# Kernel tuning notes

Hardware: AMD Instinct MI355X
Metric: run time of the kernel (lower is better)

Reference implementation:

```python
import jax, jax.numpy as jnp
import numpy as np

B, N, D = 8, 256, 64  # batch, n_entities, feature dim


def setup_inputs() -> dict:
    key = jax.random.key(0)
    ks = jax.random.split(key, 8)
    s = 0.02
    return {
        "emb1": jax.random.normal(ks[0], (B, N, D), jnp.float32),
        "emb2": jax.random.normal(ks[1], (B, N, N, D), jnp.float32),
        "W1a": jax.random.normal(ks[2], (3 * D, 128), jnp.float32) * s,
        "b1a": jnp.zeros((128,), jnp.float32),
        "W1b": jax.random.normal(ks[3], (128, D), jnp.float32) * s,
        "b1b": jnp.zeros((D,), jnp.float32),
        "W2a": jax.random.normal(ks[4], (4 * D, 256), jnp.float32) * s,
        "b2a": jnp.zeros((256,), jnp.float32),
        "W2b": jax.random.normal(ks[5], (256, D), jnp.float32) * s,
        "b2b": jnp.zeros((D,), jnp.float32),
    }


def _mlp(x, Wa, ba, Wb, bb):
    h = jax.nn.relu(jnp.einsum("...i,io->...o", x, Wa) + ba)
    return jnp.einsum("...i,io->...o", h, Wb) + bb


def reference(emb1, emb2, W1a, b1a, W1b, b1b, W2a, b2a, W2b, b2b):
    # arity 1: reduce arity-2 embedding over second entity dim (max & min), concat
    red_max = jnp.max(emb2, axis=-2)           # [B,N,D]
    red_min = jnp.min(emb2, axis=-2)           # [B,N,D]
    cat1 = jnp.concatenate([emb1, red_max, red_min], axis=-1)  # [B,N,3D]

    # arity 2: expand arity-1 embedding along a new entity dim, concat with emb2
    exp = jnp.broadcast_to(emb1[:, :, None, :], emb2.shape)    # [B,N,N,D]
    cat2 = jnp.concatenate([exp, emb2], axis=-1)               # [B,N,N,2D]

    # permutation gather: position (i,j) gets [cat2[j,i], cat2[i,j]] along features
    perm2 = jnp.concatenate([jnp.transpose(cat2, (0, 2, 1, 3)), cat2], axis=-1)  # [B,N,N,4D]

    out1 = _mlp(cat1, W1a, b1a, W1b, b1b)    # [B,N,D]
    out2 = _mlp(perm2, W2a, b2a, W2b, b2b)   # [B,N,N,D]
    return (out1, out2)
```

## Files before the change

### kernel.cpp

```cpp
#include <hip/hip_runtime.h>
#include <hip/hip_bf16.h>

typedef __bf16 bf16x8 __attribute__((ext_vector_type(8)));
typedef float f32x4 __attribute__((ext_vector_type(4)));
typedef unsigned int u32;
typedef unsigned short u16;
typedef u32 u32x4 __attribute__((ext_vector_type(4)));
typedef u16 u16x4 __attribute__((ext_vector_type(4)));
typedef u16 u16x8 __attribute__((ext_vector_type(8)));

__device__ __forceinline__ u16 f2bf(float x) {
  u32 u = __float_as_uint(x);
  return (u16)((u + 0x7FFFu + ((u >> 16) & 1u)) >> 16);
}
__device__ __forceinline__ u16 cvt_bf16(float x) {
  __bf16 h = (__bf16)x;
  return __builtin_bit_cast(u16, h);
}
__device__ __forceinline__ float bf2f(u16 h) {
  return __uint_as_float((u32)h << 16);
}

__device__ __forceinline__ bf16x8 ld_frag_lds(const u16* base, int byteOff) {
  u32x4 v = *(const u32x4*)((const char*)base + byteOff);
  return __builtin_bit_cast(bf16x8, v);
}
__device__ __forceinline__ bf16x8 ld_frag_glb(const u16* p) {
  u32x4 v = *(const u32x4*)p;
  return __builtin_bit_cast(bf16x8, v);
}

__global__ void prep_w_kernel(const float* __restrict__ W2a, const float* __restrict__ W2b,
                              u16* __restrict__ wfA, u16* __restrict__ wfB2) {
  int t = blockIdx.x * 256 + threadIdx.x;
  if (t < 8192) {
    int lane = t & 63;
    int ks = (t >> 6) & 7;
    int ntg = t >> 9;
    int col = (ntg << 4) + (lane & 15);
    int kb = (ks << 5) + ((lane >> 4) << 3);
#pragma unroll
    for (int q = 0; q < 8; ++q)
      wfA[t * 8 + q] = f2bf(W2a[(kb + q) * 256 + col]);
  } else if (t < 10240) {
    int t2i = t - 8192;
    int lane = t2i & 63;
    int dt = (t2i >> 6) & 3;
    int tt = (t2i >> 8) & 1;
    int w = t2i >> 9;
    int g = lane >> 4, c = lane & 15;
    int col = (dt << 4) + c;
#pragma unroll
    for (int q = 0; q < 8; ++q) {
      int pi = (q < 4) ? (g * 4 + q) : (16 + g * 4 + (q - 4));
      int n = w * 64 + tt * 32 + pi;
      wfB2[t2i * 8 + q] = f2bf(W2b[n * 64 + col]);
    }
  }
}

__global__ __launch_bounds__(256) void out1_kernel(
    const float* __restrict__ emb1, const float* __restrict__ emb2,
    const float* __restrict__ W1a, const float* __restrict__ b1a,
    const float* __restrict__ W1b, const float* __restrict__ b1b,
    float* __restrict__ out1) {
  int bi = blockIdx.x;
  int t = threadIdx.x;
  __shared__ float smax[4][64];
  __shared__ float smin[4][64];
  __shared__ float cat1[192];
  __shared__ float h[128];

  int d = t & 63, q = t >> 6;
  const float* base = emb2 + (size_t)bi * 256 * 64;
  float vmax = -INFINITY, vmin = INFINITY;
  for (int j = q; j < 256; j += 4) {
    float v = base[j * 64 + d];
    vmax = fmaxf(vmax, v);
    vmin = fminf(vmin, v);
  }
  smax[q][d] = vmax;
  smin[q][d] = vmin;
  __syncthreads();
  if (t < 64) {
    float mx = fmaxf(fmaxf(smax[0][t], smax[1][t]), fmaxf(smax[2][t], smax[3][t]));
    float mn = fminf(fminf(smin[0][t], smin[1][t]), fminf(smin[2][t], smin[3][t]));
    cat1[t] = emb1[bi * 64 + t];
    cat1[64 + t] = mx;
    cat1[128 + t] = mn;
  }
  __syncthreads();
  if (t < 128) {
    float acc = b1a[t];
    for (int k = 0; k < 192; ++k) acc += cat1[k] * W1a[k * 128 + t];
    h[t] = fmaxf(acc, 0.f);
  }
  __syncthreads();
  if (t < 64) {
    float acc = b1b[t];
    for (int k = 0; k < 128; ++k) acc += h[k] * W1b[k * 64 + t];
    out1[bi * 64 + t] = acc;
  }
}

__global__ __launch_bounds__(256, 2) void out2_kernel(
    const float* __restrict__ emb1, const float* __restrict__ emb2,
    const float* __restrict__ b2a, const float* __restrict__ b2b,
    const u16* __restrict__ wfA, const u16* __restrict__ wfB2,
    float* __restrict__ out2) {
  __shared__ __align__(16) u16 SH[16384];

  int blk = blockIdx.x;
  int b = blk >> 10;
  int i = (blk >> 2) & 255;
  int j0 = (blk & 3) << 6;
  int t = threadIdx.x;
  int lane = t & 63;
  int w = t >> 6;
  int lr = lane & 15;
  int lg = lane >> 4;

  {
    int r = t >> 2;
    int c16 = (t & 3) << 4;
    const float* s0 = emb1 + ((b << 8) + j0 + r) * 64;
    const float* s1 = emb2 + ((((size_t)(b << 8) + j0 + r) << 8) + i) * 64;
    const float* s2 = emb1 + ((b << 8) + i) * 64;
    const float* s3 = emb2 + ((((size_t)(b << 8) + i) << 8) + (j0 + r)) * 64;
    const float* srcs[4] = {s0, s1, s2, s3};
#pragma unroll
    for (int seg = 0; seg < 4; ++seg) {
      const float* src = srcs[seg];
#pragma unroll
      for (int u = 0; u < 2; ++u) {
        int d = c16 + (u << 3);
        float4 v0 = *(const float4*)(src + d);
        float4 v1 = *(const float4*)(src + d + 4);
        u16x8 o = {cvt_bf16(v0.x), cvt_bf16(v0.y), cvt_bf16(v0.z), cvt_bf16(v0.w),
                   cvt_bf16(v1.x), cvt_bf16(v1.y), cvt_bf16(v1.z), cvt_bf16(v1.w)};
        int byteOff = (r * 512 + ((seg << 6) + d) * 2) ^ ((r & 7) << 4);
        *(u16x8*)((char*)SH + byteOff) = o;
      }
    }
  }
  __syncthreads();

  f32x4 acc1[4][4];
#pragma unroll
  for (int m = 0; m < 4; ++m)
#pragma unroll
    for (int nt = 0; nt < 4; ++nt) acc1[m][nt] = (f32x4){0.f, 0.f, 0.f, 0.f};

  bf16x8 aF[2][4], bF[2][4];
#pragma unroll
  for (int nt = 0; nt < 4; ++nt)
    bF[0][nt] = ld_frag_glb(wfA + (size_t)((((w << 2) + nt) * 8 + 0) * 64 + lane) * 8);
#pragma unroll
  for (int m = 0; m < 4; ++m)
    aF[0][m] = ld_frag_lds(SH, (((m << 4) + lr) * 512 + (lg << 4)) ^ ((lr & 7) << 4));

#pragma unroll
  for (int ks = 0; ks < 8; ++ks) {
    const int cur = ks & 1;
    const int nxt = cur ^ 1;
    if (ks < 7) {
      int kByte = ((ks + 1) << 6) + (lg << 4);
#pragma unroll
      for (int nt = 0; nt < 4; ++nt)
        bF[nxt][nt] = ld_frag_glb(wfA + (size_t)((((w << 2) + nt) * 8 + (ks + 1)) * 64 + lane) * 8);
#pragma unroll
      for (int m = 0; m < 4; ++m)
        aF[nxt][m] = ld_frag_lds(SH, (((m << 4) + lr) * 512 + kByte) ^ ((lr & 7) << 4));
    }
#pragma unroll
    for (int m = 0; m < 4; ++m)
#pragma unroll
      for (int nt = 0; nt < 4; ++nt)
        acc1[m][nt] = __builtin_amdgcn_mfma_f32_16x16x32_bf16(bF[cur][nt], aF[cur][m],
                                                              acc1[m][nt], 0, 0, 0);
  }

  __syncthreads();

  bf16x8 wfb[8];
#pragma unroll
  for (int t2 = 0; t2 < 2; ++t2)
#pragma unroll
    for (int dt = 0; dt < 4; ++dt)
      wfb[t2 * 4 + dt] =
          ld_frag_glb(wfB2 + (size_t)(((((w << 1) + t2) << 2) + dt) * 64 + lane) * 8);

  f32x4 acc2[4][4];
#pragma unroll
  for (int m = 0; m < 4; ++m)
#pragma unroll
    for (int dt = 0; dt < 4; ++dt) acc2[m][dt] = (f32x4){0.f, 0.f, 0.f, 0.f};

#pragma unroll
  for (int t2 = 0; t2 < 2; ++t2) {
    int nbase = (w << 6) + (t2 << 5) + (lg << 2);
    float4 ba = *(const float4*)(b2a + nbase);
    float4 bb = *(const float4*)(b2a + nbase + 16);
    bf16x8 h[4];
#pragma unroll
    for (int m = 0; m < 4; ++m) {
      f32x4 pa = acc1[m][2 * t2];
      f32x4 pb = acc1[m][2 * t2 + 1];
      u16x8 hp = {cvt_bf16(fmaxf(pa[0] + ba.x, 0.f)), cvt_bf16(fmaxf(pa[1] + ba.y, 0.f)),
                  cvt_bf16(fmaxf(pa[2] + ba.z, 0.f)), cvt_bf16(fmaxf(pa[3] + ba.w, 0.f)),
                  cvt_bf16(fmaxf(pb[0] + bb.x, 0.f)), cvt_bf16(fmaxf(pb[1] + bb.y, 0.f)),
                  cvt_bf16(fmaxf(pb[2] + bb.z, 0.f)), cvt_bf16(fmaxf(pb[3] + bb.w, 0.f))};
      h[m] = __builtin_bit_cast(bf16x8, hp);
    }
#pragma unroll
    for (int dt = 0; dt < 4; ++dt) {
#pragma unroll
      for (int m = 0; m < 4; ++m)
        acc2[m][dt] = __builtin_amdgcn_mfma_f32_16x16x32_bf16(wfb[t2 * 4 + dt], h[m],
                                                              acc2[m][dt], 0, 0, 0);
    }
  }

  char* red = (char*)SH;
#pragma unroll
  for (int dt = 0; dt < 4; ++dt) {
    if (dt != w) {
      int s = dt - (dt > w ? 1 : 0);
#pragma unroll
      for (int m = 0; m < 4; ++m) {
        f32x4 p = acc2[m][dt];
        u16x4 o = {cvt_bf16(p[0]), cvt_bf16(p[1]), cvt_bf16(p[2]), cvt_bf16(p[3])};
        *(u16x4*)(red + (((w * 12 + s * 4 + m) << 9) + (lane << 3))) = o;
      }
    }
  }
  __syncthreads();

  f32x4 accO[4];
#pragma unroll
  for (int m = 0; m < 4; ++m) {
    accO[m] = acc2[m][0];
#pragma unroll
    for (int dt = 1; dt < 4; ++dt)
      if (w == dt) accO[m] = acc2[m][dt];
  }
#pragma unroll
  for (int wp = 0; wp < 4; ++wp) {
    if (wp != w) {
      int s = w - (w > wp ? 1 : 0);
#pragma unroll
      for (int m = 0; m < 4; ++m) {
        u16x4 o = *(const u16x4*)(red + (((wp * 12 + s * 4 + m) << 9) + (lane << 3)));
        accO[m][0] += bf2f(o[0]);
        accO[m][1] += bf2f(o[1]);
        accO[m][2] += bf2f(o[2]);
        accO[m][3] += bf2f(o[3]);
      }
    }
  }

  float4 bias2 = *(const float4*)(b2b + (w << 4) + (lg << 2));
  float* obase = out2 + (((size_t)(b << 8) + i) * 256 + j0) * 64 + (w << 4) + (lg << 2);
#pragma unroll
  for (int m = 0; m < 4; ++m) {
    float4 v = {accO[m][0] + bias2.x, accO[m][1] + bias2.y,
                accO[m][2] + bias2.z, accO[m][3] + bias2.w};
    *(float4*)(obase + (size_t)((m << 4) + lr) * 64) = v;
  }
}

extern "C" void kernel_launch(void* const* d_in, const int* in_sizes, int n_in,
                              void* d_out, int out_size, void* d_ws, size_t ws_size,
                              hipStream_t stream) {
  const float* emb1 = (const float*)d_in[0];
  const float* emb2 = (const float*)d_in[1];
  const float* W1a  = (const float*)d_in[2];
  const float* b1a  = (const float*)d_in[3];
  const float* W1b  = (const float*)d_in[4];
  const float* b1b  = (const float*)d_in[5];
  const float* W2a  = (const float*)d_in[6];
  const float* b2a  = (const float*)d_in[7];
  const float* W2b  = (const float*)d_in[8];
  const float* b2b  = (const float*)d_in[9];

  float* out = (float*)d_out;
  u16* wfA  = (u16*)d_ws;
  u16* wfB2 = wfA + 65536;

  prep_w_kernel<<<40, 256, 0, stream>>>(W2a, W2b, wfA, wfB2);
  out1_kernel<<<2048, 256, 0, stream>>>(emb1, emb2, W1a, b1a, W1b, b1b, out);
  out2_kernel<<<8192, 256, 0, stream>>>(emb1, emb2, b2a, b2b, wfA, wfB2,
                                        out + 8 * 256 * 64);
}
```

Measured before the change: 152.6 us.

## Pre-convert embeddings to bf16 and stage tiles via direct global-to-LDS loads

out1_kernel now also writes a bf16 copy of emb2 while it computes the max/min reduction, and a new small kernel converts emb1 to bf16. A new out2 kernel then loads its input tiles from these bf16 copies with global_load_lds, going straight to shared memory without register staging or in-kernel conversion. This halves the bytes out2 reads, but adds a 64 MB bf16 write of emb2 plus an extra launch. The new path only runs when the workspace is large enough; otherwise the old path is used.

Measured after the change: 173.1 us. 1.13x slower.

```diff
diff --git a/kernel.cpp b/kernel.cpp
--- a/kernel.cpp
+++ b/kernel.cpp
@@ -59,11 +59,22 @@
   }
 }
 
+__global__ __launch_bounds__(256) void prep_e1_kernel(const float* __restrict__ emb1,
+                                                      u16* __restrict__ e1b) {
+  int t = blockIdx.x * 256 + threadIdx.x;
+  const float* p = emb1 + t * 8;
+  float4 a0 = *(const float4*)p;
+  float4 a1 = *(const float4*)(p + 4);
+  u16x8 o = {f2bf(a0.x), f2bf(a0.y), f2bf(a0.z), f2bf(a0.w),
+             f2bf(a1.x), f2bf(a1.y), f2bf(a1.z), f2bf(a1.w)};
+  *(u16x8*)(e1b + t * 8) = o;
+}
+
 __global__ __launch_bounds__(256) void out1_kernel(
     const float* __restrict__ emb1, const float* __restrict__ emb2,
     const float* __restrict__ W1a, const float* __restrict__ b1a,
     const float* __restrict__ W1b, const float* __restrict__ b1b,
-    float* __restrict__ out1) {
+    float* __restrict__ out1, u16* __restrict__ e2b) {
   int bi = blockIdx.x;
   int t = threadIdx.x;
   __shared__ float smax[4][64];
@@ -74,10 +85,20 @@
   int d = t & 63, q = t >> 6;
   const float* base = emb2 + (size_t)bi * 256 * 64;
   float vmax = -INFINITY, vmin = INFINITY;
-  for (int j = q; j < 256; j += 4) {
-    float v = base[j * 64 + d];
-    vmax = fmaxf(vmax, v);
-    vmin = fminf(vmin, v);
+  if (e2b) {
+    u16* eb = e2b + (size_t)bi * 256 * 64;
+    for (int j = q; j < 256; j += 4) {
+      float v = base[j * 64 + d];
+      eb[j * 64 + d] = f2bf(v);
+      vmax = fmaxf(vmax, v);
+      vmin = fminf(vmin, v);
+    }
+  } else {
+    for (int j = q; j < 256; j += 4) {
+      float v = base[j * 64 + d];
+      vmax = fmaxf(vmax, v);
+      vmin = fminf(vmin, v);
+    }
   }
   smax[q][d] = vmax;
   smin[q][d] = vmin;
@@ -103,8 +124,13 @@
   }
 }
 
-__global__ __launch_bounds__(256, 2) void out2_kernel(
-    const float* __restrict__ emb1, const float* __restrict__ emb2,
+__device__ __forceinline__ int xoff(int ks, int m, int lr, int lg) {
+  int inner = (((m << 4) + lr) << 7) + ((ks & 1) << 6) + (lg << 4);
+  return ((ks >> 1) << 13) + (inner ^ ((lr & 7) << 4));
+}
+
+__global__ __launch_bounds__(256, 2) void out2_dma_kernel(
+    const u16* __restrict__ e1b, const u16* __restrict__ e2b,
     const float* __restrict__ b2a, const float* __restrict__ b2b,
     const u16* __restrict__ wfA, const u16* __restrict__ wfB2,
     float* __restrict__ out2) {
@@ -121,6 +147,165 @@
   int lg = lane >> 4;
 
   {
+    int rsub = lane >> 3;
+    int slot = lane & 7;
+    int cb = ((slot ^ rsub) << 4);
+#pragma unroll
+    for (int c = 0; c < 8; ++c) {
+      int r = (c << 3) + rsub;
+      const u16* srow;
+      if (w == 0)      srow = e1b + (((b << 8) + j0 + r) << 6);
+      else if (w == 1) srow = e2b + ((((size_t)(b << 8) + j0 + r) << 8) + i) * 64;
+      else if (w == 2) srow = e1b + (((b << 8) + i) << 6);
+      else             srow = e2b + ((((size_t)(b << 8) + i) << 8) + (j0 + r)) * 64;
+      __builtin_amdgcn_global_load_lds(
+          (const __attribute__((address_space(1))) u32*)((const char*)srow + cb),
+          (__attribute__((address_space(3))) u32*)((char*)SH + (w << 13) + (c << 10)),
+          16, 0, 0);
+    }
+  }
+  __syncthreads();
+
+  f32x4 acc1[4][4];
+#pragma unroll
+  for (int m = 0; m < 4; ++m)
+#pragma unroll
+    for (int nt = 0; nt < 4; ++nt) acc1[m][nt] = (f32x4){0.f, 0.f, 0.f, 0.f};
+
+  bf16x8 aF[2][4], bF[2][4];
+#pragma unroll
+  for (int nt = 0; nt < 4; ++nt)
+    bF[0][nt] = ld_frag_glb(wfA + (size_t)((((w << 2) + nt) * 8 + 0) * 64 + lane) * 8);
+#pragma unroll
+  for (int m = 0; m < 4; ++m)
+    aF[0][m] = ld_frag_lds(SH, xoff(0, m, lr, lg));
+
+#pragma unroll
+  for (int ks = 0; ks < 8; ++ks) {
+    const int cur = ks & 1;
+    const int nxt = cur ^ 1;
+    if (ks < 7) {
+#pragma unroll
+      for (int nt = 0; nt < 4; ++nt)
+        bF[nxt][nt] = ld_frag_glb(wfA + (size_t)((((w << 2) + nt) * 8 + (ks + 1)) * 64 + lane) * 8);
+#pragma unroll
+      for (int m = 0; m < 4; ++m)
+        aF[nxt][m] = ld_frag_lds(SH, xoff(ks + 1, m, lr, lg));
+    }
+#pragma unroll
+    for (int m = 0; m < 4; ++m)
+#pragma unroll
+      for (int nt = 0; nt < 4; ++nt)
+        acc1[m][nt] = __builtin_amdgcn_mfma_f32_16x16x32_bf16(bF[cur][nt], aF[cur][m],
+                                                              acc1[m][nt], 0, 0, 0);
+  }
+
+  __syncthreads();
+
+  bf16x8 wfb[8];
+#pragma unroll
+  for (int t2 = 0; t2 < 2; ++t2)
+#pragma unroll
+    for (int dt = 0; dt < 4; ++dt)
+      wfb[t2 * 4 + dt] =
+          ld_frag_glb(wfB2 + (size_t)(((((w << 1) + t2) << 2) + dt) * 64 + lane) * 8);
+
+  f32x4 acc2[4][4];
+#pragma unroll
+  for (int m = 0; m < 4; ++m)
+#pragma unroll
+    for (int dt = 0; dt < 4; ++dt) acc2[m][dt] = (f32x4){0.f, 0.f, 0.f, 0.f};
+
+#pragma unroll
+  for (int t2 = 0; t2 < 2; ++t2) {
+    int nbase = (w << 6) + (t2 << 5) + (lg << 2);
+    float4 ba = *(const float4*)(b2a + nbase);
+    float4 bb = *(const float4*)(b2a + nbase + 16);
+    bf16x8 h[4];
+#pragma unroll
+    for (int m = 0; m < 4; ++m) {
+      f32x4 pa = acc1[m][2 * t2];
+      f32x4 pb = acc1[m][2 * t2 + 1];
+      u16x8 hp = {cvt_bf16(fmaxf(pa[0] + ba.x, 0.f)), cvt_bf16(fmaxf(pa[1] + ba.y, 0.f)),
+                  cvt_bf16(fmaxf(pa[2] + ba.z, 0.f)), cvt_bf16(fmaxf(pa[3] + ba.w, 0.f)),
+                  cvt_bf16(fmaxf(pb[0] + bb.x, 0.f)), cvt_bf16(fmaxf(pb[1] + bb.y, 0.f)),
+                  cvt_bf16(fmaxf(pb[2] + bb.z, 0.f)), cvt_bf16(fmaxf(pb[3] + bb.w, 0.f))};
+      h[m] = __builtin_bit_cast(bf16x8, hp);
+    }
+#pragma unroll
+    for (int dt = 0; dt < 4; ++dt)
+#pragma unroll
+      for (int m = 0; m < 4; ++m)
+        acc2[m][dt] = __builtin_amdgcn_mfma_f32_16x16x32_bf16(wfb[t2 * 4 + dt], h[m],
+                                                              acc2[m][dt], 0, 0, 0);
+  }
+
+  char* red = (char*)SH;
+#pragma unroll
+  for (int dt = 0; dt < 4; ++dt) {
+    if (dt != w) {
+      int s = dt - (dt > w ? 1 : 0);
+#pragma unroll
+      for (int m = 0; m < 4; ++m) {
+        f32x4 p = acc2[m][dt];
+        u16x4 o = {cvt_bf16(p[0]), cvt_bf16(p[1]), cvt_bf16(p[2]), cvt_bf16(p[3])};
+        *(u16x4*)(red + (((w * 12 + s * 4 + m) << 9) + (lane << 3))) = o;
+      }
+    }
+  }
+  __syncthreads();
+
+  f32x4 accO[4];
+#pragma unroll
+  for (int m = 0; m < 4; ++m) {
+    accO[m] = acc2[m][0];
+#pragma unroll
+    for (int dt = 1; dt < 4; ++dt)
+      if (w == dt) accO[m] = acc2[m][dt];
+  }
+#pragma unroll
+  for (int wp = 0; wp < 4; ++wp) {
+    if (wp != w) {
+      int s = w - (w > wp ? 1 : 0);
+#pragma unroll
+      for (int m = 0; m < 4; ++m) {
+        u16x4 o = *(const u16x4*)(red + (((wp * 12 + s * 4 + m) << 9) + (lane << 3)));
+        accO[m][0] += bf2f(o[0]);
+        accO[m][1] += bf2f(o[1]);
+        accO[m][2] += bf2f(o[2]);
+        accO[m][3] += bf2f(o[3]);
+      }
+    }
+  }
+
+  float4 bias2 = *(const float4*)(b2b + (w << 4) + (lg << 2));
+  float* obase = out2 + (((size_t)(b << 8) + i) * 256 + j0) * 64 + (w << 4) + (lg << 2);
+#pragma unroll
+  for (int m = 0; m < 4; ++m) {
+    float4 v = {accO[m][0] + bias2.x, accO[m][1] + bias2.y,
+                accO[m][2] + bias2.z, accO[m][3] + bias2.w};
+    *(float4*)(obase + (size_t)((m << 4) + lr) * 64) = v;
+  }
+}
+
+__global__ __launch_bounds__(256, 2) void out2_kernel(
+    const float* __restrict__ emb1, const float* __restrict__ emb2,
+    const float* __restrict__ b2a, const float* __restrict__ b2b,
+    const u16* __restrict__ wfA, const u16* __restrict__ wfB2,
+    float* __restrict__ out2) {
+  __shared__ __align__(16) u16 SH[16384];
+
+  int blk = blockIdx.x;
+  int b = blk >> 10;
+  int i = (blk >> 2) & 255;
+  int j0 = (blk & 3) << 6;
+  int t = threadIdx.x;
+  int lane = t & 63;
+  int w = t >> 6;
+  int lr = lane & 15;
+  int lg = lane >> 4;
+
+  {
     int r = t >> 2;
     int c16 = (t & 3) << 4;
     const float* s0 = emb1 + ((b << 8) + j0 + r) * 64;
@@ -213,12 +398,11 @@
       h[m] = __builtin_bit_cast(bf16x8, hp);
     }
 #pragma unroll
-    for (int dt = 0; dt < 4; ++dt) {
+    for (int dt = 0; dt < 4; ++dt)
 #pragma unroll
       for (int m = 0; m < 4; ++m)
         acc2[m][dt] = __builtin_amdgcn_mfma_f32_16x16x32_bf16(wfb[t2 * 4 + dt], h[m],
                                                               acc2[m][dt], 0, 0, 0);
-    }
   }
 
   char* red = (char*)SH;
@@ -286,9 +470,22 @@
   float* out = (float*)d_out;
   u16* wfA  = (u16*)d_ws;
   u16* wfB2 = wfA + 65536;
+  u16* e1b  = wfB2 + 16384;
+  u16* e2b  = e1b + 131072;
+  size_t need = ((size_t)65536 + 16384 + 131072 + 33554432) * 2;
+  bool dma = ws_size >= need;
 
   prep_w_kernel<<<40, 256, 0, stream>>>(W2a, W2b, wfA, wfB2);
-  out1_kernel<<<2048, 256, 0, stream>>>(emb1, emb2, W1a, b1a, W1b, b1b, out);
-  out2_kernel<<<8192, 256, 0, stream>>>(emb1, emb2, b2a, b2b, wfA, wfB2,
-                                        out + 8 * 256 * 64);
-}
+  if (dma) {
+    prep_e1_kernel<<<64, 256, 0, stream>>>(emb1, e1b);
+    out1_kernel<<<2048, 256, 0, stream>>>(emb1, emb2, W1a, b1a, W1b, b1b,
+                                          out, e2b);
+    out2_dma_kernel<<<8192, 256, 0, stream>>>(e1b, e2b, b2a, b2b, wfA, wfB2,
+                                              out + 8 * 256 * 64);
+  } else {
+    out1_kernel<<<2048, 256, 0, stream>>>(emb1, emb2, W1a, b1a, W1b, b1b,
+                                          out, nullptr);
+    out2_kernel<<<8192, 256, 0, stream>>>(emb1, emb2, b2a, b2b, wfA, wfB2,
+                                          out + 8 * 256 * 64);
+  }
+}
```
